# Performance work log

Hardware: AMD Instinct MI355X
Metric: run time of the kernel (lower is better)

The kernel has to match this reference:

```python
import jax, jax.numpy as jnp
import numpy as np

CODEBOOK_SIZE = 8192
LATENT_DIM = 512
DECAY = 0.99
COMMITMENT_COST = 0.25
EPS = 1e-5


def setup_inputs() -> dict:
    key = jax.random.key(0)
    k1, k2, k3 = jax.random.split(key, 3)
    z = jax.random.normal(k1, (8, 2048, LATENT_DIM), dtype=jnp.float32)
    # nn.init.uniform_(-1/K, 1/K) style small init
    embedding = jax.random.normal(k2, (CODEBOOK_SIZE, LATENT_DIM), dtype=jnp.float32) / CODEBOOK_SIZE
    ema_cluster_size = jnp.ones((CODEBOOK_SIZE,), dtype=jnp.float32)
    ema_embed_sum = embedding.copy()
    del k3
    return {
        "z": z,
        "embedding": embedding,
        "ema_cluster_size": ema_cluster_size,
        "ema_embed_sum": ema_embed_sum,
    }


def reference(z, embedding, ema_cluster_size, ema_embed_sum):
    B, T, D = z.shape
    K = embedding.shape[0]
    flat_z = z.reshape(-1, D)  # (N, D), N = B*T

    # squared L2 distances: ||z||^2 - 2 z.E^T + ||E||^2  -> (N, K)
    dist = (
        jnp.sum(flat_z * flat_z, axis=-1, keepdims=True)
        - 2.0 * flat_z @ embedding.T
        + jnp.sum(embedding * embedding, axis=-1)
    )
    indices_flat = jnp.argmin(dist, axis=-1)  # (N,)
    indices = indices_flat.reshape(B, T)

    z_q = embedding[indices_flat].reshape(B, T, D)

    # EMA update (training mode; one_hot.sum / one_hot.T @ z == segment sums)
    new_cluster_size = jax.ops.segment_sum(
        jnp.ones_like(indices_flat, dtype=jnp.float32), indices_flat, num_segments=K
    )
    new_embed_sum = jax.ops.segment_sum(flat_z, indices_flat, num_segments=K)
    ema_cs = ema_cluster_size * DECAY + new_cluster_size * (1.0 - DECAY)
    ema_es = ema_embed_sum * DECAY + new_embed_sum * (1.0 - DECAY)
    n = jnp.sum(ema_cs)
    smoothed = (ema_cs + EPS) / (n + K * EPS) * n
    new_embedding = ema_es / smoothed[:, None]

    # commitment loss (codebook side is handled by EMA, z_q detached)
    loss = COMMITMENT_COST * jnp.mean((jax.lax.stop_gradient(z_q) - z) ** 2)

    # straight-through estimator
    z_q_st = z + jax.lax.stop_gradient(z_q - z)

    return z_q_st, loss, indices, new_embedding, ema_cs, ema_es
```

## Files before the change

### kernel.cpp

```cpp
#include <hip/hip_runtime.h>
#include <hip/hip_bf16.h>
#include <math.h>

#define K_CODES 8192
#define D_DIM   512
#define N_ROWS  16384
#define DECAYF  0.99f
#define OMDF    0.01f
#define COMMIT  0.25f
#define EPSV    1e-5f

#define OUT0_OFF 0ull
#define OUT1_OFF 8388608ull
#define OUT2_OFF 8388609ull
#define OUT3_OFF 8404993ull
#define OUT4_OFF 12599297ull
#define OUT5_OFF 12607489ull

#define BM 128
#define BN 256
#define BKC 32
#define NRB (N_ROWS / BM)
#define NCB (K_CODES / BN)
#define NITER (D_DIM / BKC)
#define NLBUCK 512

typedef _Float16 f16x8 __attribute__((ext_vector_type(8)));
typedef _Float16 f16x4 __attribute__((ext_vector_type(4)));
typedef float    f32x4 __attribute__((ext_vector_type(4)));
typedef unsigned short u16;

#define GLOAD16(srcp, dstp) __builtin_amdgcn_global_load_lds( \
    (const __attribute__((address_space(1))) unsigned int*)(const void*)(srcp), \
    (__attribute__((address_space(3))) unsigned int*)(void*)(dstp), 16, 0, 0)

__device__ __forceinline__ void pack_tile(const float* __restrict__ src,
                                          u16* __restrict__ dst, float scale,
                                          int pb, int t, int tid,
                                          u16 (*simg)[1024][8]) {
    const float4* base = (const float4*)(src + ((size_t)pb * 256) * D_DIM + t * 32);
#pragma unroll
    for (int i = 0; i < 8; i++) {
        int f = tid + i * 256;
        int r = f >> 3, c = f & 7;
        float4 v = base[(size_t)r * 128 + c];
        float s0 = v.x * scale, s1 = v.y * scale, s2 = v.z * scale, s3 = v.w * scale;
        _Float16 h0 = (_Float16)s0, h1 = (_Float16)s1, h2 = (_Float16)s2, h3 = (_Float16)s3;
        f16x4 hv = {h0, h1, h2, h3};
        f16x4 lv = {(_Float16)(s0 - (float)h0), (_Float16)(s1 - (float)h1),
                    (_Float16)(s2 - (float)h2), (_Float16)(s3 - (float)h3)};
        int slot = (c >> 1) * 256 + r;
        int half = (c & 1) * 4;
        *(f16x4*)&simg[0][slot][half] = hv;
        *(f16x4*)&simg[1][slot][half] = lv;
    }
    __syncthreads();
    const u16* flat = &simg[0][0][0];
    u16* gout = dst + ((size_t)pb * 16 + t) * 2 * 8192;
#pragma unroll
    for (int i = 0; i < 8; i++) {
        int g = tid + i * 256;
        *(f16x8*)(gout + (size_t)g * 8) = *(const f16x8*)(flat + (size_t)g * 8);
    }
}

__device__ __forceinline__ void norms8(const float* __restrict__ src,
                                       float* __restrict__ dst, int rowbase, int tid) {
    int lane = tid & 63;
    int wave = tid >> 6;
    int half = lane >> 5;
    int l32  = lane & 31;
    int row  = rowbase + wave * 2 + half;
    int j    = l32 & 7;
    int blk  = l32 >> 3;
    const float* p = src + (size_t)row * D_DIM + blk * 128 + j;
    float x0 = p[0];
    float r = __fmul_rn(x0, x0);
#pragma unroll
    for (int i = 1; i < 16; i++) {
        float x = p[i * 8];
        r = __fadd_rn(r, __fmul_rn(x, x));
    }
    float s1 = __fadd_rn(r,  __shfl_xor(r, 1, 64));
    float s2 = __fadd_rn(s1, __shfl_xor(s1, 2, 64));
    float s4 = __fadd_rn(s2, __shfl_xor(s2, 4, 64));
    float t1 = __fadd_rn(s4, __shfl_xor(s4, 8, 64));
    float t2 = __fadd_rn(t1, __shfl_xor(t1, 16, 64));
    if (l32 == 0) dst[row] = t2;
}

__global__ void prep_kernel(const float* __restrict__ z, const float* __restrict__ E,
                            u16* __restrict__ zpack, u16* __restrict__ epack,
                            float* __restrict__ z2, float* __restrict__ e2,
                            int* __restrict__ cnt, float* __restrict__ lossbuf) {
    __shared__ __align__(16) u16 simg[2][1024][8];
    int bid = blockIdx.x;
    int tid = threadIdx.x;
    if (bid < 1024) {
        pack_tile(z, zpack, 1.0f, bid >> 4, bid & 15, tid, simg);
    } else if (bid < 1536) {
        int b = bid - 1024;
        pack_tile(E, epack, 4096.0f, b >> 4, b & 15, tid, simg);
    } else if (bid < 3584) {
        norms8(z, z2, (bid - 1536) * 8, tid);
    } else if (bid < 4608) {
        norms8(E, e2, (bid - 3584) * 8, tid);
    } else {
#pragma unroll
        for (int i = 0; i < 32; i++) cnt[tid + i * 256] = 0;
        lossbuf[tid] = 0.f;
        lossbuf[tid + 256] = 0.f;
    }
}

__global__ __launch_bounds__(512, 4) void argmin_mfma_kernel(
    const u16* __restrict__ zpack, const u16* __restrict__ epack,
    const float* __restrict__ e2, const float* __restrict__ z2,
    float* __restrict__ pv, int* __restrict__ pi)
{
    __shared__ __align__(16) u16 ldsA[2][512][8];
    __shared__ __align__(16) u16 ldsB[2][2][1024][8];

    int bid = blockIdx.x;
    int xcd = bid & 7, sub = bid >> 3;
    int rb  = sub >> 2;
    int cb  = xcd * 4 + (sub & 3);
    int row0 = rb * BM, col0 = cb * BN;
    int pb   = rb >> 1, phalf = rb & 1;

    int tid = threadIdx.x;
    int l   = tid & 63;
    int w   = tid >> 6;
    int mw  = w >> 2, nw = w & 3;
    int lg  = l >> 4;
    int l16 = l & 15;

    f32x4 acc[4][4];
#pragma unroll
    for (int m = 0; m < 4; m++)
#pragma unroll
        for (int n = 0; n < 4; n++)
            acc[m][n] = (f32x4){0.f, 0.f, 0.f, 0.f};

    auto stageA = [&](int t) {
        const u16* zb = zpack + (((size_t)pb * 16 + t) * 2) * 8192;
#pragma unroll
        for (int i = 0; i < 2; i++) {
            int idx = tid + i * 512;
            int p = idx >> 9, rem = idx & 511;
            int g = rem >> 7, r = rem & 127;
            GLOAD16(zb + ((size_t)p * 1024 + g * 256 + phalf * 128 + r) * 8,
                    &ldsA[p][g * 128 + r][0]);
        }
    };
    auto stageB = [&](int buf, int t) {
        const u16* eb = epack + (((size_t)cb * 16 + t) * 2) * 8192;
#pragma unroll
        for (int i = 0; i < 2; i++) {
            int slot = tid + i * 512;
            GLOAD16(eb + (size_t)slot * 8,        &ldsB[buf][0][slot][0]);
            GLOAD16(eb + 8192 + (size_t)slot * 8, &ldsB[buf][1][slot][0]);
        }
    };

    stageB(0, 0);

    for (int t = 0; t < NITER; t++) {
        int cur = t & 1;
        asm volatile("s_waitcnt lgkmcnt(0)" ::: "memory");
        __builtin_amdgcn_s_barrier();
        asm volatile("" ::: "memory");

        stageA(t);
        if (t + 1 < NITER) stageB(cur ^ 1, t + 1);

        if (t + 1 < NITER) { asm volatile("s_waitcnt vmcnt(4)" ::: "memory"); }
        else               { asm volatile("s_waitcnt vmcnt(0)" ::: "memory"); }
        __builtin_amdgcn_s_barrier();
        asm volatile("" ::: "memory");

        f16x8 bh[4], bl[4];
#pragma unroll
        for (int n = 0; n < 4; n++) {
            int s = lg * 256 + nw * 64 + n * 16 + l16;
            bh[n] = *(const f16x8*)&ldsB[cur][0][s][0];
            bl[n] = *(const f16x8*)&ldsB[cur][1][s][0];
        }
#pragma unroll
        for (int m = 0; m < 4; m++) {
            int s = lg * 128 + mw * 64 + m * 16 + l16;
            f16x8 ah = *(const f16x8*)&ldsA[0][s][0];
            f16x8 al = *(const f16x8*)&ldsA[1][s][0];
#pragma unroll
            for (int n = 0; n < 4; n++)
                acc[m][n] = __builtin_amdgcn_mfma_f32_16x16x32_f16(ah, bh[n], acc[m][n], 0, 0, 0);
#pragma unroll
            for (int n = 0; n < 4; n++)
                acc[m][n] = __builtin_amdgcn_mfma_f32_16x16x32_f16(ah, bl[n], acc[m][n], 0, 0, 0);
#pragma unroll
            for (int n = 0; n < 4; n++)
                acc[m][n] = __builtin_amdgcn_mfma_f32_16x16x32_f16(al, bh[n], acc[m][n], 0, 0, 0);
        }
    }

    const float nscale = -0.00048828125f;
    float e2c[4];
#pragma unroll
    for (int n = 0; n < 4; n++) e2c[n] = e2[col0 + nw * 64 + n * 16 + l16];

    __syncthreads();
    float* redv = (float*)&ldsA[0][0][0];
    int*   redi = (int*)&ldsB[0][0][0][0];

#pragma unroll
    for (int m = 0; m < 4; m++) {
#pragma unroll
        for (int r = 0; r < 4; r++) {
            int rl = mw * 64 + m * 16 + lg * 4 + r;
            float z2v = z2[row0 + rl];
            float bv = 1e30f; int bc = 0x7fffffff;
#pragma unroll
            for (int n = 0; n < 4; n++) {
                int code = col0 + nw * 64 + n * 16 + l16;
                float v = __fadd_rn(__fadd_rn(z2v, __fmul_rn(acc[m][n][r], nscale)), e2c[n]);
                if (v < bv) { bv = v; bc = code; }
            }
#pragma unroll
            for (int s = 1; s < 16; s <<= 1) {
                float ov = __shfl_xor(bv, s, 64);
                int   oc = __shfl_xor(bc, s, 64);
                if (ov < bv || (ov == bv && oc < bc)) { bv = ov; bc = oc; }
            }
            if (l16 == r) {
                redv[rl * 4 + nw] = bv;
                redi[rl * 4 + nw] = bc;
            }
        }
    }
    __syncthreads();
    if (tid < BM) {
        float bv = redv[tid * 4]; int bc = redi[tid * 4];
#pragma unroll
        for (int q = 1; q < 4; q++) {
            float v = redv[tid * 4 + q]; int c = redi[tid * 4 + q];
            if (v < bv || (v == bv && c < bc)) { bv = v; bc = c; }
        }
        pv[(size_t)(row0 + tid) * NCB + cb] = bv;
        pi[(size_t)(row0 + tid) * NCB + cb] = bc;
    }
}

__global__ void combine_gather_kernel(const float* __restrict__ pv, const int* __restrict__ pi,
                                      const float* __restrict__ z, const float* __restrict__ E,
                                      int* __restrict__ idx_out, float* __restrict__ out2,
                                      int* __restrict__ cnt, float* __restrict__ out0,
                                      float* __restrict__ lossbuf) {
    int row = blockIdx.x;
    int t = threadIdx.x;
    __shared__ int ksh;
    if (t < 32) {
        float bv = pv[(size_t)row * NCB + t];
        int   bc = pi[(size_t)row * NCB + t];
#pragma unroll
        for (int s = 1; s < 32; s <<= 1) {
            float ov = __shfl_xor(bv, s, 64);
            int   oc = __shfl_xor(bc, s, 64);
            if (ov < bv || (ov == bv && oc < bc)) { bv = ov; bc = oc; }
        }
        if (t == 0) {
            idx_out[row] = bc;
            out2[row] = (float)bc;
            atomicAdd(&cnt[bc], 1);
            ksh = bc;
        }
    }
    __syncthreads();
    int k = ksh;
    int d = t * 4;
    float4 zv = *(const float4*)(z + (size_t)row * D_DIM + d);
    float4 qv = *(const float4*)(E + (size_t)k * D_DIM + d);
    float4 o;
    o.x = __fadd_rn(zv.x, __fsub_rn(qv.x, zv.x));
    o.y = __fadd_rn(zv.y, __fsub_rn(qv.y, zv.y));
    o.z = __fadd_rn(zv.z, __fsub_rn(qv.z, zv.z));
    o.w = __fadd_rn(zv.w, __fsub_rn(qv.w, zv.w));
    *(float4*)(out0 + (size_t)row * D_DIM + d) = o;
    float dx = qv.x - zv.x, dy = qv.y - zv.y, dz = qv.z - zv.z, dw = qv.w - zv.w;
    float s = dx * dx + dy * dy + dz * dz + dw * dw;
#pragma unroll
    for (int off = 32; off; off >>= 1) s += __shfl_down(s, off, 64);
    __shared__ float part[2];
    if ((t & 63) == 0) part[t >> 6] = s;
    __syncthreads();
    if (t == 0) atomicAdd(&lossbuf[row & (NLBUCK - 1)], part[0] + part[1]);
}

__global__ void mid_kernel(const int* __restrict__ cnt, int* __restrict__ offs,
                           const int* __restrict__ idx, int* __restrict__ rowlist,
                           const float* __restrict__ cs, float* __restrict__ s_in,
                           const float* __restrict__ lossbuf, float* __restrict__ out1) {
    __shared__ int loc_offs[K_CODES];
    __shared__ int sums[1024];
    __shared__ float fpart[16];
    int t = threadIdx.x;
    int base = t * 8;
    int loc[8]; int s = 0;
#pragma unroll
    for (int i = 0; i < 8; i++) { loc[i] = s; s += cnt[base + i]; }
    sums[t] = s;
    __syncthreads();
    for (int off = 1; off < 1024; off <<= 1) {
        int v = (t >= off) ? sums[t - off] : 0;
        __syncthreads();
        sums[t] += v;
        __syncthreads();
    }
    int excl = sums[t] - s;
#pragma unroll
    for (int i = 0; i < 8; i++) loc_offs[base + i] = excl + loc[i];
    __syncthreads();
#pragma unroll
    for (int i = 0; i < 16; i++) {
        int row = i * 1024 + t;
        int k = idx[row];
        int pos = atomicAdd(&loc_offs[k], 1);
        rowlist[pos] = row;
    }
    __syncthreads();
#pragma unroll
    for (int i = 0; i < 8; i++) offs[base + i] = loc_offs[base + i];
    float fs = 0.f;
    for (int i = t; i < K_CODES; i += 1024) fs += cs[i];
#pragma unroll
    for (int off = 32; off; off >>= 1) fs += __shfl_down(fs, off, 64);
    if ((t & 63) == 0) fpart[t >> 6] = fs;
    __syncthreads();
    if (t == 0) {
        float tot = 0.f;
#pragma unroll
        for (int i = 0; i < 16; i++) tot += fpart[i];
        s_in[0] = tot;
    }
    __syncthreads();
    float ls = (t < NLBUCK) ? lossbuf[t] : 0.f;
#pragma unroll
    for (int off = 32; off; off >>= 1) ls += __shfl_down(ls, off, 64);
    if ((t & 63) == 0) fpart[t >> 6] = ls;
    __syncthreads();
    if (t == 0) {
        float tot = 0.f;
#pragma unroll
        for (int i = 0; i < 16; i++) tot += fpart[i];
        out1[0] = COMMIT * tot / (float)(N_ROWS * D_DIM);
    }
}

__global__ void cluster_kernel(const float* __restrict__ z, const float* __restrict__ in_cs,
                               const float* __restrict__ in_es, const int* __restrict__ cnt,
                               const int* __restrict__ offs_end, const int* __restrict__ rowlist,
                               const float* __restrict__ s_in,
                               float* __restrict__ out3, float* __restrict__ out4,
                               float* __restrict__ out5) {
    int k = blockIdx.x;
    int t = threadIdx.x;
    int c = cnt[k];
    int end = offs_end[k];
    int start = end - c;
    int d = t * 4;
    float ax = 0.f, ay = 0.f, az = 0.f, aw = 0.f;
    for (int i = 0; i < c; i++) {
        int row = rowlist[start + i];
        float4 zv = *(const float4*)(z + (size_t)row * D_DIM + d);
        ax += zv.x; ay += zv.y; az += zv.z; aw += zv.w;
    }
    float ema_cs = DECAYF * in_cs[k] + OMDF * (float)c;
    float n = DECAYF * s_in[0] + OMDF * (float)N_ROWS;
    float smoothed = (ema_cs + EPSV) / (n + (float)K_CODES * EPSV) * n;
    float4 esv = *(const float4*)(in_es + (size_t)k * D_DIM + d);
    float4 ema;
    ema.x = DECAYF * esv.x + OMDF * ax;
    ema.y = DECAYF * esv.y + OMDF * ay;
    ema.z = DECAYF * esv.z + OMDF * az;
    ema.w = DECAYF * esv.w + OMDF * aw;
    *(float4*)(out5 + (size_t)k * D_DIM + d) = ema;
    float4 emb;
    emb.x = ema.x / smoothed;
    emb.y = ema.y / smoothed;
    emb.z = ema.z / smoothed;
    emb.w = ema.w / smoothed;
    *(float4*)(out3 + (size_t)k * D_DIM + d) = emb;
    if (t == 0) out4[k] = ema_cs;
}

extern "C" void kernel_launch(void* const* d_in, const int* in_sizes, int n_in,
                              void* d_out, int out_size, void* d_ws, size_t ws_size,
                              hipStream_t stream) {
    const float* z     = (const float*)d_in[0];
    const float* E     = (const float*)d_in[1];
    const float* in_cs = (const float*)d_in[2];
    const float* in_es = (const float*)d_in[3];

    float* out  = (float*)d_out;
    float* out0 = out + OUT0_OFF;
    float* out1 = out + OUT1_OFF;
    float* out2 = out + OUT2_OFF;
    float* out3 = out + OUT3_OFF;
    float* out4 = out + OUT4_OFF;
    float* out5 = out + OUT5_OFF;

    u16* zpack = (u16*)out0;
    u16* epack = (u16*)(out + OUT3_OFF + 3);
    float* pv = out5;
    int*   pi = (int*)(out5 + (size_t)NCB * N_ROWS);

    char* ws = (char*)d_ws;
    float* e2      = (float*)(ws);
    float* z2      = (float*)(ws + 32 * 1024);
    int*   idxb    = (int*)  (ws + 96 * 1024);
    int*   cnt     = (int*)  (ws + 160 * 1024);
    int*   offs    = (int*)  (ws + 192 * 1024);
    int*   rowlist = (int*)  (ws + 224 * 1024);
    float* lossbuf = (float*)(ws + 288 * 1024);
    float* s_in    = (float*)(ws + 292 * 1024);

    prep_kernel<<<4609, 256, 0, stream>>>(z, E, zpack, epack, z2, e2, cnt, lossbuf);
    argmin_mfma_kernel<<<NRB * NCB, 512, 0, stream>>>(zpack, epack, e2, z2, pv, pi);
    combine_gather_kernel<<<N_ROWS, 128, 0, stream>>>(pv, pi, z, E, idxb, out2, cnt,
                                                      out0, lossbuf);
    mid_kernel<<<1, 1024, 0, stream>>>(cnt, offs, idxb, rowlist, in_cs, s_in,
                                       lossbuf, out1);
    cluster_kernel<<<K_CODES, 128, 0, stream>>>(z, in_cs, in_es, cnt, offs, rowlist,
                                                s_in, out3, out4, out5);
}
```

Measured before the change: 454.4 us.

## Enlarge argmin GEMM tile to 256x256 with phased prefetch and priority scheduling

```diff
diff --git a/kernel.cpp b/kernel.cpp
--- a/kernel.cpp
+++ b/kernel.cpp
@@ -17,12 +17,11 @@
 #define OUT4_OFF 12599297ull
 #define OUT5_OFF 12607489ull
 
-#define BM 128
+#define BM 256
 #define BN 256
-#define BKC 32
 #define NRB (N_ROWS / BM)
 #define NCB (K_CODES / BN)
-#define NITER (D_DIM / BKC)
+#define NITER 16
 #define NLBUCK 512
 
 typedef _Float16 f16x8 __attribute__((ext_vector_type(8)));
@@ -113,20 +112,18 @@
     }
 }
 
-__global__ __launch_bounds__(512, 4) void argmin_mfma_kernel(
+__global__ __launch_bounds__(512, 1) void argmin_mfma_kernel(
     const u16* __restrict__ zpack, const u16* __restrict__ epack,
     const float* __restrict__ e2, const float* __restrict__ z2,
     float* __restrict__ pv, int* __restrict__ pi)
 {
-    __shared__ __align__(16) u16 ldsA[2][512][8];
-    __shared__ __align__(16) u16 ldsB[2][2][1024][8];
+    __shared__ __align__(16) u16 lds[2][4][1024][8];
 
     int bid = blockIdx.x;
     int xcd = bid & 7, sub = bid >> 3;
     int rb  = sub >> 2;
     int cb  = xcd * 4 + (sub & 3);
     int row0 = rb * BM, col0 = cb * BN;
-    int pb   = rb >> 1, phalf = rb & 1;
 
     int tid = threadIdx.x;
     int l   = tid & 63;
@@ -135,71 +132,73 @@
     int lg  = l >> 4;
     int l16 = l & 15;
 
-    f32x4 acc[4][4];
-#pragma unroll
-    for (int m = 0; m < 4; m++)
+    f32x4 acc[8][4];
+#pragma unroll
+    for (int m = 0; m < 8; m++)
 #pragma unroll
         for (int n = 0; n < 4; n++)
             acc[m][n] = (f32x4){0.f, 0.f, 0.f, 0.f};
 
-    auto stageA = [&](int t) {
-        const u16* zb = zpack + (((size_t)pb * 16 + t) * 2) * 8192;
-#pragma unroll
-        for (int i = 0; i < 2; i++) {
-            int idx = tid + i * 512;
-            int p = idx >> 9, rem = idx & 511;
-            int g = rem >> 7, r = rem & 127;
-            GLOAD16(zb + ((size_t)p * 1024 + g * 256 + phalf * 128 + r) * 8,
-                    &ldsA[p][g * 128 + r][0]);
-        }
+    auto stage_half = [&](int buf, int t, int i) {
+        const u16* zb = zpack + (((size_t)rb * 16 + t) * 2) * 8192;
+        const u16* eb = epack + (((size_t)cb * 16 + t) * 2) * 8192;
+        int slot = tid + i * 512;
+        GLOAD16(zb + (size_t)slot * 8,        &lds[buf][0][slot][0]);
+        GLOAD16(zb + 8192 + (size_t)slot * 8, &lds[buf][1][slot][0]);
+        GLOAD16(eb + (size_t)slot * 8,        &lds[buf][2][slot][0]);
+        GLOAD16(eb + 8192 + (size_t)slot * 8, &lds[buf][3][slot][0]);
     };
-    auto stageB = [&](int buf, int t) {
-        const u16* eb = epack + (((size_t)cb * 16 + t) * 2) * 8192;
-#pragma unroll
-        for (int i = 0; i < 2; i++) {
-            int slot = tid + i * 512;
-            GLOAD16(eb + (size_t)slot * 8,        &ldsB[buf][0][slot][0]);
-            GLOAD16(eb + 8192 + (size_t)slot * 8, &ldsB[buf][1][slot][0]);
-        }
-    };
-
-    stageB(0, 0);
+
+    stage_half(0, 0, 0);
+    stage_half(0, 0, 1);
 
     for (int t = 0; t < NITER; t++) {
         int cur = t & 1;
-        asm volatile("s_waitcnt lgkmcnt(0)" ::: "memory");
+        asm volatile("s_waitcnt vmcnt(0)" ::: "memory");
         __builtin_amdgcn_s_barrier();
         asm volatile("" ::: "memory");
 
-        stageA(t);
-        if (t + 1 < NITER) stageB(cur ^ 1, t + 1);
-
-        if (t + 1 < NITER) { asm volatile("s_waitcnt vmcnt(4)" ::: "memory"); }
-        else               { asm volatile("s_waitcnt vmcnt(0)" ::: "memory"); }
-        __builtin_amdgcn_s_barrier();
-        asm volatile("" ::: "memory");
-
         f16x8 bh[4], bl[4];
 #pragma unroll
-        for (int n = 0; n < 4; n++) {
-            int s = lg * 256 + nw * 64 + n * 16 + l16;
-            bh[n] = *(const f16x8*)&ldsB[cur][0][s][0];
-            bl[n] = *(const f16x8*)&ldsB[cur][1][s][0];
-        }
-#pragma unroll
-        for (int m = 0; m < 4; m++) {
-            int s = lg * 128 + mw * 64 + m * 16 + l16;
-            f16x8 ah = *(const f16x8*)&ldsA[0][s][0];
-            f16x8 al = *(const f16x8*)&ldsA[1][s][0];
-#pragma unroll
-            for (int n = 0; n < 4; n++)
-                acc[m][n] = __builtin_amdgcn_mfma_f32_16x16x32_f16(ah, bh[n], acc[m][n], 0, 0, 0);
-#pragma unroll
-            for (int n = 0; n < 4; n++)
-                acc[m][n] = __builtin_amdgcn_mfma_f32_16x16x32_f16(ah, bl[n], acc[m][n], 0, 0, 0);
-#pragma unroll
-            for (int n = 0; n < 4; n++)
-                acc[m][n] = __builtin_amdgcn_mfma_f32_16x16x32_f16(al, bh[n], acc[m][n], 0, 0, 0);
+        for (int p = 0; p < 4; p++) {
+            if (p == 0) {
+#pragma unroll
+                for (int n = 0; n < 4; n++) {
+                    int s = lg * 256 + nw * 64 + n * 16 + l16;
+                    bh[n] = *(const f16x8*)&lds[cur][2][s][0];
+                    bl[n] = *(const f16x8*)&lds[cur][3][s][0];
+                }
+            }
+            f16x8 ah[2], al[2];
+#pragma unroll
+            for (int mm = 0; mm < 2; mm++) {
+                int s = lg * 256 + mw * 128 + (p * 2 + mm) * 16 + l16;
+                ah[mm] = *(const f16x8*)&lds[cur][0][s][0];
+                al[mm] = *(const f16x8*)&lds[cur][1][s][0];
+            }
+            if (p < 2 && t + 1 < NITER) stage_half(cur ^ 1, t + 1, p);
+
+            __builtin_amdgcn_s_barrier();
+            asm volatile("s_waitcnt lgkmcnt(0)" ::: "memory");
+            __builtin_amdgcn_sched_barrier(0);
+            __builtin_amdgcn_s_setprio(1);
+#pragma unroll
+            for (int mm = 0; mm < 2; mm++) {
+                int m = p * 2 + mm;
+#pragma unroll
+                for (int n = 0; n < 4; n++)
+                    acc[m][n] = __builtin_amdgcn_mfma_f32_16x16x32_f16(ah[mm], bh[n], acc[m][n], 0, 0, 0);
+#pragma unroll
+                for (int n = 0; n < 4; n++)
+                    acc[m][n] = __builtin_amdgcn_mfma_f32_16x16x32_f16(ah[mm], bl[n], acc[m][n], 0, 0, 0);
+#pragma unroll
+                for (int n = 0; n < 4; n++)
+                    acc[m][n] = __builtin_amdgcn_mfma_f32_16x16x32_f16(al[mm], bh[n], acc[m][n], 0, 0, 0);
+            }
+            __builtin_amdgcn_s_setprio(0);
+            asm volatile("" ::: "memory");
+            __builtin_amdgcn_s_barrier();
+            asm volatile("" ::: "memory");
         }
     }
 
@@ -208,15 +207,14 @@
 #pragma unroll
     for (int n = 0; n < 4; n++) e2c[n] = e2[col0 + nw * 64 + n * 16 + l16];
 
-    __syncthreads();
-    float* redv = (float*)&ldsA[0][0][0];
-    int*   redi = (int*)&ldsB[0][0][0][0];
-
-#pragma unroll
-    for (int m = 0; m < 4; m++) {
+    float* redv = (float*)&lds[0][0][0][0];
+    int*   redi = (int*)((char*)redv + 4096);
+
+#pragma unroll
+    for (int m = 0; m < 8; m++) {
 #pragma unroll
         for (int r = 0; r < 4; r++) {
-            int rl = mw * 64 + m * 16 + lg * 4 + r;
+            int rl = mw * 128 + m * 16 + lg * 4 + r;
             float z2v = z2[row0 + rl];
             float bv = 1e30f; int bc = 0x7fffffff;
 #pragma unroll
```

Result: slower. 503.2 us (+10.8%).
